# Kernel tuning notes

Measured on AMD Instinct MI355X. Metric: run time of the kernel, lower is better.

## Reference

```python
import jax, jax.numpy as jnp
import numpy as np
import math

V = 1_000_000  # number of mesh vertices
J = 23         # number of joints (fixed by kintree_table in source)
PARENTS = np.array([-1, 0, 1, 1, 3, 4, 5, 4, 7, 4, 9, 1, 11, 12, 13, 12, 15, 12, 17, 0, 19, 0, 21])


def setup_inputs() -> dict:
    key = jax.random.key(0)
    ks = jax.random.split(key, 16)
    v_template = jax.random.normal(ks[0], (1, V, 3), jnp.float32) * 0.5
    w = jax.random.uniform(ks[1], (1, V, J), jnp.float32)
    skinning = w / w.sum(-1, keepdims=True)  # rows sum to 1 like LBS weights
    joints_rest = jax.random.normal(ks[2], (1, J, 3), jnp.float32) * 0.3
    jp = lambda i: jax.random.normal(ks[3 + i], (1, 3), jnp.float32) * 0.1
    return {
        'v_template': v_template,
        'skinning': skinning,
        'joints_rest': joints_rest,
        'joint_0': jp(0), 'joint_1': jp(1), 'joint_2': jp(2), 'joint_3': jp(3),
        'joint_4': jp(4), 'joint_5': jp(5), 'joint_12': jp(6), 'joint_13': jp(7),
        'local_adjust': jax.random.normal(ks[11], (1, V, 3), jnp.float32) * 0.01,
        'displacement': jax.random.normal(ks[12], (1, 1, 3), jnp.float32) * 0.01,
        'scale': jnp.ones((1,), jnp.float32),
        'estimated_location': jax.random.normal(ks[13], (1, 3), jnp.float32),
        'batch_size': 4,
    }


def rodrigues(r):
    # r: [J,3] axis-angle -> [J,3,3] rotation matrices
    angle = jnp.sqrt(jnp.sum(r * r, axis=-1, keepdims=True) + 1e-12)  # [J,1]
    axis = r / angle
    x, y, z = axis[:, 0], axis[:, 1], axis[:, 2]
    zero = jnp.zeros_like(x)
    K = jnp.stack([zero, -z, y, z, zero, -x, -y, x, zero], axis=-1).reshape(-1, 3, 3)
    s = jnp.sin(angle)[..., None]
    c = jnp.cos(angle)[..., None]
    I = jnp.eye(3, dtype=r.dtype)
    return I + s * K + (1.0 - c) * (K @ K)


def build_pose_tensor(joint_0, joint_1, joint_2, joint_3, joint_4, joint_5, joint_12, joint_13):
    pi = math.pi
    pose = jnp.zeros((J, 3), jnp.float32)
    pose = pose.at[0].set(pi / 2 * jnp.tanh(joint_0[0]))
    pose = pose.at[1].set(pi / 4 * jnp.tanh(joint_1[0]))
    pose = pose.at[2].set(pi / 9 * jnp.tanh(joint_2[0]))
    pose = pose.at[3].set(pi / 3 * jnp.tanh(joint_3[0]))
    pose = pose.at[11].set(pi / 3 * jnp.tanh(joint_3[0]) * jnp.array([1.0, -1.0, -1.0], jnp.float32))
    pose = pose.at[4].set(pi / 3 * jnp.tanh(joint_4[0]))
    pose = pose.at[12].set(pi / 3 * jnp.tanh(joint_12[0]))
    pose = pose.at[13].set(pi / 3 * jnp.tanh(joint_13[0]))
    pose = pose.at[5].set(pi / 3 * jnp.tanh(joint_5[0]))
    return pose


def lbs(verts, joints, pose):
    # verts: [V,3], joints: [J,3], pose: [J,3] axis-angle
    R = rodrigues(pose)  # [J,3,3]
    rel = joints.at[1:].add(-joints[PARENTS[1:]])  # parent-relative joint offsets
    # local 4x4 transforms
    T_local = jnp.zeros((J, 4, 4), verts.dtype)
    T_local = T_local.at[:, :3, :3].set(R)
    T_local = T_local.at[:, :3, 3].set(rel)
    T_local = T_local.at[:, 3, 3].set(1.0)
    # compose along kinematic tree (fixed 23-joint chain -> small static loop)
    G = [T_local[0]]
    for j in range(1, J):
        G.append(G[PARENTS[j]] @ T_local[j])
    G = jnp.stack(G)  # [J,4,4]
    posed_joints = G[:, :3, 3]
    # remove rest-pose joint locations: A = G * [[I,-j],[0,1]]
    t_corr = jnp.einsum('jab,jb->ja', G[:, :3, :3], joints)
    A = G.at[:, :3, 3].add(-t_corr)  # [J,4,4]
    # skin vertices: per-vertex blended transform
    T = (skinning_ref[0] @ A.reshape(J, 16)).reshape(-1, 4, 4) if False else None
    return A, posed_joints


def reference(v_template, skinning, joints_rest, joint_0, joint_1, joint_2, joint_3,
              joint_4, joint_5, joint_12, joint_13, local_adjust, displacement,
              scale, estimated_location, batch_size):
    pose = build_pose_tensor(joint_0, joint_1, joint_2, joint_3, joint_4, joint_5,
                             joint_12, joint_13)
    verts = v_template[0] + 0.1 * jnp.tanh(local_adjust[0])  # [V,3]
    joints = joints_rest[0]  # [J,3]
    A, posed_joints = lbs(verts, joints, pose)
    # weighted per-vertex transforms: [V,J] @ [J,16] -> [V,4,4]  (memory-bound)
    Tv = (skinning[0] @ A.reshape(J, 16)).reshape(-1, 4, 4)
    v_h = jnp.concatenate([verts, jnp.ones((verts.shape[0], 1), verts.dtype)], axis=-1)
    verts_posed = jnp.einsum('vab,vb->va', Tv, v_h)[:, :3]  # [V,3]
    disp = 0.1 * jnp.tanh(displacement[0, 0])  # [3]
    loc = estimated_location[0]  # [3]
    verts_out = 0.0035 * scale[0] * verts_posed + loc + disp  # [V,3]
    joints_out = 0.0035 * scale[0] * posed_joints + loc + disp  # [J,3]
    verts_batched = jnp.broadcast_to(verts_out[None], (batch_size,) + verts_out.shape)
    return verts_batched, pose, joints_out, scale, displacement, local_adjust
```

## Files before the change

kernel.cpp:

```cpp
#include <hip/hip_runtime.h>

#define V_N 1000000
#define J_N 23
#define BLK 256

#define OUT_POSE   12000000
#define OUT_JOINTS 12000069
#define OUT_SCALE  12000138
#define OUT_DISP   12000139
#define OUT_LA     12000142

__device__ __constant__ int c_parents[J_N] = {
    -1, 0, 1, 1, 3, 4, 5, 4, 7, 4, 9, 1, 11, 12, 13, 12, 15, 12, 17, 0, 19, 0, 21
};

__global__ void stage1_kernel(
    const float* __restrict__ joints_rest,
    const float* __restrict__ j0, const float* __restrict__ j1,
    const float* __restrict__ j2, const float* __restrict__ j3,
    const float* __restrict__ j4, const float* __restrict__ j5,
    const float* __restrict__ j12, const float* __restrict__ j13,
    const float* __restrict__ disp, const float* __restrict__ scale,
    const float* __restrict__ loc,
    float* __restrict__ wsA, float* __restrict__ out)
{
    __shared__ float jr[J_N][3];
    __shared__ float pose[J_N][3];
    __shared__ float R[J_N][9];
    __shared__ float rel[J_N][3];
    __shared__ float G[J_N][12];
    __shared__ float sb[4];
    const int t = threadIdx.x;

    if (t < J_N * 3) {
        ((float*)jr)[t]   = joints_rest[t];
        ((float*)pose)[t] = 0.0f;
    }
    __syncthreads();

    if (t < 27) {
        const float PI = 3.14159265358979323846f;
        const int   rows[9] = { 0, 1, 2, 3, 11, 4, 5, 12, 13 };
        const float cf[9]   = { PI/2, PI/4, PI/9, PI/3, PI/3, PI/3, PI/3, PI/3, PI/3 };
        int i = t / 3, cmp = t % 3;
        const float* srcs[9];
        srcs[0]=j0; srcs[1]=j1; srcs[2]=j2; srcs[3]=j3; srcs[4]=j3;
        srcs[5]=j4; srcs[6]=j5; srcs[7]=j12; srcs[8]=j13;
        float syz = (rows[i] == 11 && cmp > 0) ? -1.0f : 1.0f;
        pose[rows[i]][cmp] = cf[i] * syz * tanhf(srcs[i][cmp]);
    }
    if (t == 32) {
        sb[0] = 0.0035f * scale[0];
        sb[1] = loc[0] + 0.1f * tanhf(disp[0]);
        sb[2] = loc[1] + 0.1f * tanhf(disp[1]);
        sb[3] = loc[2] + 0.1f * tanhf(disp[2]);
    }
    __syncthreads();

    if (t < J_N) {
        float rx = pose[t][0], ry = pose[t][1], rz = pose[t][2];
        float ang = sqrtf(rx*rx + ry*ry + rz*rz + 1e-12f);
        float inv = 1.0f / ang;
        float x = rx * inv, y = ry * inv, z = rz * inv;
        float s = sinf(ang), c = cosf(ang);
        float K[9]  = { 0.f, -z, y,  z, 0.f, -x,  -y, x, 0.f };
        float K2[9];
        for (int r = 0; r < 3; r++)
            for (int cc = 0; cc < 3; cc++) {
                float a = 0.f;
                for (int k = 0; k < 3; k++) a += K[r*3+k] * K[k*3+cc];
                K2[r*3+cc] = a;
            }
        for (int r = 0; r < 3; r++)
            for (int cc = 0; cc < 3; cc++) {
                float id = (r == cc) ? 1.f : 0.f;
                R[t][r*3+cc] = id + s * K[r*3+cc] + (1.f - c) * K2[r*3+cc];
            }
        int p = c_parents[t];
        for (int cc = 0; cc < 3; cc++)
            rel[t][cc] = (p < 0) ? jr[t][cc] : (jr[t][cc] - jr[p][cc]);
    }
    __syncthreads();

    if (t == 0) {
        for (int r = 0; r < 3; r++) {
            for (int cc = 0; cc < 3; cc++) G[0][r*4+cc] = R[0][r*3+cc];
            G[0][r*4+3] = rel[0][r];
        }
        for (int j = 1; j < J_N; j++) {
            int p = c_parents[j];
            for (int r = 0; r < 3; r++) {
                float g0 = G[p][r*4+0], g1 = G[p][r*4+1], g2 = G[p][r*4+2], g3 = G[p][r*4+3];
                for (int cc = 0; cc < 3; cc++)
                    G[j][r*4+cc] = g0*R[j][0*3+cc] + g1*R[j][1*3+cc] + g2*R[j][2*3+cc];
                G[j][r*4+3] = g0*rel[j][0] + g1*rel[j][1] + g2*rel[j][2] + g3;
            }
        }
    }
    __syncthreads();

    if (t < J_N) {
        for (int r = 0; r < 3; r++) {
            float tc = G[t][r*4+0]*jr[t][0] + G[t][r*4+1]*jr[t][1] + G[t][r*4+2]*jr[t][2];
            wsA[t*12 + r*4 + 0] = G[t][r*4+0];
            wsA[t*12 + r*4 + 1] = G[t][r*4+1];
            wsA[t*12 + r*4 + 2] = G[t][r*4+2];
            wsA[t*12 + r*4 + 3] = G[t][r*4+3] - tc;
            out[OUT_JOINTS + t*3 + r] = sb[0] * G[t][r*4+3] + sb[1+r];
        }
    }
    if (t < J_N * 3) out[OUT_POSE + t] = ((const float*)pose)[t];
    if (t == 0) {
        wsA[276] = sb[0]; wsA[277] = sb[1]; wsA[278] = sb[2]; wsA[279] = sb[3];
        out[OUT_SCALE]  = scale[0];
        out[OUT_DISP+0] = disp[0]; out[OUT_DISP+1] = disp[1]; out[OUT_DISP+2] = disp[2];
    }
}

__global__ void stage2_kernel(
    const float* __restrict__ vt,
    const float* __restrict__ skin,
    const float* __restrict__ la,
    const float* __restrict__ wsA,
    const int* __restrict__ bsp,
    float* __restrict__ out)
{
    const int v = blockIdx.x * BLK + threadIdx.x;
    if (v >= V_N) return;

    const float* wp = skin + (size_t)v * J_N;
    float w[J_N];
    #pragma unroll
    for (int j = 0; j < J_N; j++) w[j] = wp[j];

    const float* vp = vt + (size_t)v * 3;
    const float* lp = la + (size_t)v * 3;
    const float cvx = vp[0], cvy = vp[1], cvz = vp[2];
    const float clx = lp[0], cly = lp[1], clz = lp[2];

    const float vx = cvx + 0.1f * tanhf(clx);
    const float vy = cvy + 0.1f * tanhf(cly);
    const float vz = cvz + 0.1f * tanhf(clz);

    float acc[12];
    #pragma unroll
    for (int k = 0; k < 12; k++) acc[k] = 0.f;
    #pragma unroll
    for (int j = 0; j < J_N; j++) {
        const float wj = w[j];
        const float* Aj = wsA + j * 12;
        #pragma unroll
        for (int k = 0; k < 12; k++) acc[k] = fmaf(wj, Aj[k], acc[k]);
    }

    const float px = acc[0]*vx + acc[1]*vy + acc[2]*vz  + acc[3];
    const float py = acc[4]*vx + acc[5]*vy + acc[6]*vz  + acc[7];
    const float pz = acc[8]*vx + acc[9]*vy + acc[10]*vz + acc[11];
    const float sc = wsA[276];
    const float ox = fmaf(sc, px, wsA[277]);
    const float oy = fmaf(sc, py, wsA[278]);
    const float oz = fmaf(sc, pz, wsA[279]);

    const int bsz = bsp[0];
    float* ob = out + (size_t)v * 3;
    for (int b = 0; b < bsz; b++) {
        ob[0] = ox; ob[1] = oy; ob[2] = oz;
        ob += 3000000;
    }
    float* oe = out + OUT_LA + (size_t)v * 3;
    oe[0] = clx; oe[1] = cly; oe[2] = clz;
}

extern "C" void kernel_launch(void* const* d_in, const int* in_sizes, int n_in,
                              void* d_out, int out_size, void* d_ws, size_t ws_size,
                              hipStream_t stream) {
    const float* vt   = (const float*)d_in[0];
    const float* skin = (const float*)d_in[1];
    const float* jr   = (const float*)d_in[2];
    const float* j0   = (const float*)d_in[3];
    const float* j1   = (const float*)d_in[4];
    const float* j2   = (const float*)d_in[5];
    const float* j3   = (const float*)d_in[6];
    const float* j4   = (const float*)d_in[7];
    const float* j5   = (const float*)d_in[8];
    const float* j12  = (const float*)d_in[9];
    const float* j13  = (const float*)d_in[10];
    const float* la   = (const float*)d_in[11];
    const float* disp = (const float*)d_in[12];
    const float* sc   = (const float*)d_in[13];
    const float* loc  = (const float*)d_in[14];
    const int* bs     = (const int*)d_in[15];

    float* wsA = (float*)d_ws;
    float* out = (float*)d_out;

    stage1_kernel<<<1, 128, 0, stream>>>(jr, j0, j1, j2, j3, j4, j5, j12, j13,
                                         disp, sc, loc, wsA, out);
    stage2_kernel<<<(V_N + BLK - 1) / BLK, BLK, 0, stream>>>(vt, skin, la, wsA, bs, out);
}
```

Before: 216.0 us.

## Stage skinning weights through LDS with coalesced 16-byte loads

The per-vertex kernel now uses 64-thread blocks that cooperatively load the block's contiguous skinning-weight rows as uint4 vectors into shared memory, then each thread reads its own 23 weights from LDS. Before, each thread read its own row of 23 floats with stride-23 access, which coalesces poorly. The change adds a barrier and LDS traffic with bank conflicts from the stride-23 reads, and it relies on V being an exact multiple of 64 since the bounds check was removed.

```diff
diff --git a/kernel.cpp b/kernel.cpp
--- a/kernel.cpp
+++ b/kernel.cpp
@@ -2,7 +2,8 @@
 
 #define V_N 1000000
 #define J_N 23
-#define BLK 256
+#define BLK2 64
+#define NBLK 15625
 
 #define OUT_POSE   12000000
 #define OUT_JOINTS 12000069
@@ -125,34 +126,49 @@
     const int* __restrict__ bsp,
     float* __restrict__ out)
 {
-    const int v = blockIdx.x * BLK + threadIdx.x;
-    if (v >= V_N) return;
-
-    const float* wp = skin + (size_t)v * J_N;
-    float w[J_N];
-    #pragma unroll
-    for (int j = 0; j < J_N; j++) w[j] = wp[j];
+    __shared__ uint4 s_sk[368];
+
+    const int lane = threadIdx.x;
+    const int blk  = blockIdx.x;
+    const int v    = blk * BLK2 + lane;
+
+    const uint4* g = (const uint4*)skin + (size_t)blk * 368;
+    uint4 r0 = g[lane];
+    uint4 r1 = g[lane + 64];
+    uint4 r2 = g[lane + 128];
+    uint4 r3 = g[lane + 192];
+    uint4 r4 = g[lane + 256];
+    uint4 r5 = make_uint4(0u, 0u, 0u, 0u);
+    if (lane < 48) r5 = g[lane + 320];
 
     const float* vp = vt + (size_t)v * 3;
     const float* lp = la + (size_t)v * 3;
     const float cvx = vp[0], cvy = vp[1], cvz = vp[2];
     const float clx = lp[0], cly = lp[1], clz = lp[2];
 
-    const float vx = cvx + 0.1f * tanhf(clx);
-    const float vy = cvy + 0.1f * tanhf(cly);
-    const float vz = cvz + 0.1f * tanhf(clz);
-
+    s_sk[lane]       = r0;
+    s_sk[lane + 64]  = r1;
+    s_sk[lane + 128] = r2;
+    s_sk[lane + 192] = r3;
+    s_sk[lane + 256] = r4;
+    if (lane < 48) s_sk[lane + 320] = r5;
+    __syncthreads();
+
+    const float* wr = (const float*)s_sk + lane * J_N;
     float acc[12];
     #pragma unroll
     for (int k = 0; k < 12; k++) acc[k] = 0.f;
     #pragma unroll
     for (int j = 0; j < J_N; j++) {
-        const float wj = w[j];
+        const float wj = wr[j];
         const float* Aj = wsA + j * 12;
         #pragma unroll
         for (int k = 0; k < 12; k++) acc[k] = fmaf(wj, Aj[k], acc[k]);
     }
 
+    const float vx = cvx + 0.1f * tanhf(clx);
+    const float vy = cvy + 0.1f * tanhf(cly);
+    const float vz = cvz + 0.1f * tanhf(clz);
     const float px = acc[0]*vx + acc[1]*vy + acc[2]*vz  + acc[3];
     const float py = acc[4]*vx + acc[5]*vy + acc[6]*vz  + acc[7];
     const float pz = acc[8]*vx + acc[9]*vy + acc[10]*vz + acc[11];
@@ -196,5 +212,5 @@
 
     stage1_kernel<<<1, 128, 0, stream>>>(jr, j0, j1, j2, j3, j4, j5, j12, j13,
                                          disp, sc, loc, wsA, out);
-    stage2_kernel<<<(V_N + BLK - 1) / BLK, BLK, 0, stream>>>(vt, skin, la, wsA, bs, out);
+    stage2_kernel<<<NBLK, BLK2, 0, stream>>>(vt, skin, la, wsA, bs, out);
 }
```

Result: no change. 220.1 us (+1.9%).

## Process four vertices per thread with 128-bit vector loads and nontemporal stores

Applied to the files above, without the earlier changes.

Each thread now handles four consecutive vertices. That lets it read the 92 skinning weights as 23 aligned uint4 loads, and the vertex and adjustment data as three float4 loads each. Outputs go out as vectorized nontemporal stores, 16-byte for the batched vertices and 8-byte for the local_adjust copy. The aim is fewer memory instructions and better coalescing in a kernel bound by memory bandwidth. The cost is many more registers per thread (92 weights), which lowers occupancy, and per-thread loads of 368 contiguous bytes that are strided across lanes, which may coalesce worse.

```diff
diff --git a/kernel.cpp b/kernel.cpp
--- a/kernel.cpp
+++ b/kernel.cpp
@@ -3,12 +3,16 @@
 #define V_N 1000000
 #define J_N 23
 #define BLK 256
+#define NBLK 977
 
 #define OUT_POSE   12000000
 #define OUT_JOINTS 12000069
 #define OUT_SCALE  12000138
 #define OUT_DISP   12000139
 #define OUT_LA     12000142
+
+typedef float v4f __attribute__((ext_vector_type(4)));
+typedef float v2f __attribute__((ext_vector_type(2)));
 
 __device__ __constant__ int c_parents[J_N] = {
     -1, 0, 1, 1, 3, 4, 5, 4, 7, 4, 9, 1, 11, 12, 13, 12, 15, 12, 17, 0, 19, 0, 21
@@ -125,50 +129,82 @@
     const int* __restrict__ bsp,
     float* __restrict__ out)
 {
-    const int v = blockIdx.x * BLK + threadIdx.x;
-    if (v >= V_N) return;
-
-    const float* wp = skin + (size_t)v * J_N;
-    float w[J_N];
+    const int gid = blockIdx.x * BLK + threadIdx.x;
+    const int v4  = gid << 2;
+    if (v4 >= V_N) return;
+
+    const uint4* g = (const uint4*)skin + (size_t)gid * 23;
+    uint4 wq[23];
     #pragma unroll
-    for (int j = 0; j < J_N; j++) w[j] = wp[j];
-
-    const float* vp = vt + (size_t)v * 3;
-    const float* lp = la + (size_t)v * 3;
-    const float cvx = vp[0], cvy = vp[1], cvz = vp[2];
-    const float clx = lp[0], cly = lp[1], clz = lp[2];
-
-    const float vx = cvx + 0.1f * tanhf(clx);
-    const float vy = cvy + 0.1f * tanhf(cly);
-    const float vz = cvz + 0.1f * tanhf(clz);
-
-    float acc[12];
+    for (int m = 0; m < 23; m++) wq[m] = g[m];
+
+    const float4* vp = (const float4*)(vt + (size_t)v4 * 3);
+    const float4* lp = (const float4*)(la + (size_t)v4 * 3);
+    float4 va = vp[0], vb = vp[1], vc = vp[2];
+    float4 lA = lp[0], lB = lp[1], lC = lp[2];
+
+    const float sc = wsA[276];
+    const float bx = wsA[277], by = wsA[278], bz = wsA[279];
+    const int   bsz = bsp[0];
+
+    float vv[12], ll[12];
+    vv[0]=va.x; vv[1]=va.y; vv[2] =va.z; vv[3] =va.w;
+    vv[4]=vb.x; vv[5]=vb.y; vv[6] =vb.z; vv[7] =vb.w;
+    vv[8]=vc.x; vv[9]=vc.y; vv[10]=vc.z; vv[11]=vc.w;
+    ll[0]=lA.x; ll[1]=lA.y; ll[2] =lA.z; ll[3] =lA.w;
+    ll[4]=lB.x; ll[5]=lB.y; ll[6] =lB.z; ll[7] =lB.w;
+    ll[8]=lC.x; ll[9]=lC.y; ll[10]=lC.z; ll[11]=lC.w;
+
+    const float* wf = (const float*)wq;
+
+    float o[12];
     #pragma unroll
-    for (int k = 0; k < 12; k++) acc[k] = 0.f;
-    #pragma unroll
-    for (int j = 0; j < J_N; j++) {
-        const float wj = w[j];
-        const float* Aj = wsA + j * 12;
+    for (int v = 0; v < 4; v++) {
+        float acc[12];
         #pragma unroll
-        for (int k = 0; k < 12; k++) acc[k] = fmaf(wj, Aj[k], acc[k]);
-    }
-
-    const float px = acc[0]*vx + acc[1]*vy + acc[2]*vz  + acc[3];
-    const float py = acc[4]*vx + acc[5]*vy + acc[6]*vz  + acc[7];
-    const float pz = acc[8]*vx + acc[9]*vy + acc[10]*vz + acc[11];
-    const float sc = wsA[276];
-    const float ox = fmaf(sc, px, wsA[277]);
-    const float oy = fmaf(sc, py, wsA[278]);
-    const float oz = fmaf(sc, pz, wsA[279]);
-
-    const int bsz = bsp[0];
-    float* ob = out + (size_t)v * 3;
+        for (int k = 0; k < 12; k++) acc[k] = 0.f;
+        #pragma unroll
+        for (int j = 0; j < J_N; j++) {
+            const float wj = wf[v * J_N + j];
+            const float* Aj = wsA + j * 12;
+            #pragma unroll
+            for (int k = 0; k < 12; k++) acc[k] = fmaf(wj, Aj[k], acc[k]);
+        }
+        const float vx = vv[v*3+0] + 0.1f * tanhf(ll[v*3+0]);
+        const float vy = vv[v*3+1] + 0.1f * tanhf(ll[v*3+1]);
+        const float vz = vv[v*3+2] + 0.1f * tanhf(ll[v*3+2]);
+        const float px = acc[0]*vx + acc[1]*vy + acc[2]*vz  + acc[3];
+        const float py = acc[4]*vx + acc[5]*vy + acc[6]*vz  + acc[7];
+        const float pz = acc[8]*vx + acc[9]*vy + acc[10]*vz + acc[11];
+        o[v*3+0] = fmaf(sc, px, bx);
+        o[v*3+1] = fmaf(sc, py, by);
+        o[v*3+2] = fmaf(sc, pz, bz);
+    }
+
+    v4f s0 = { o[0], o[1], o[2],  o[3] };
+    v4f s1 = { o[4], o[5], o[6],  o[7] };
+    v4f s2 = { o[8], o[9], o[10], o[11] };
     for (int b = 0; b < bsz; b++) {
-        ob[0] = ox; ob[1] = oy; ob[2] = oz;
-        ob += 3000000;
-    }
-    float* oe = out + OUT_LA + (size_t)v * 3;
-    oe[0] = clx; oe[1] = cly; oe[2] = clz;
+        v4f* ob = (v4f*)(out + (size_t)b * 3000000u + (size_t)v4 * 3);
+        __builtin_nontemporal_store(s0, ob + 0);
+        __builtin_nontemporal_store(s1, ob + 1);
+        __builtin_nontemporal_store(s2, ob + 2);
+    }
+    {
+        v2f* oe = (v2f*)((char*)out + 48000568ull + (size_t)v4 * 12u);
+        v2f e0 = { ll[0],  ll[1]  };
+        v2f e1 = { ll[2],  ll[3]  };
+        v2f e2 = { ll[4],  ll[5]  };
+        v2f e3 = { ll[6],  ll[7]  };
+        v2f e4 = { ll[8],  ll[9]  };
+        v2f e5 = { ll[10], ll[11] };
+        __builtin_nontemporal_store(e0, oe + 0);
+        __builtin_nontemporal_store(e1, oe + 1);
+        __builtin_nontemporal_store(e2, oe + 2);
+        __builtin_nontemporal_store(e3, oe + 3);
+        __builtin_nontemporal_store(e4, oe + 4);
+        __builtin_nontemporal_store(e5, oe + 5);
+    }
 }
 
 extern "C" void kernel_launch(void* const* d_in, const int* in_sizes, int n_in,
@@ -196,5 +232,5 @@
 
     stage1_kernel<<<1, 128, 0, stream>>>(jr, j0, j1, j2, j3, j4, j5, j12, j13,
                                          disp, sc, loc, wsA, out);
-    stage2_kernel<<<(V_N + BLK - 1) / BLK, BLK, 0, stream>>>(vt, skin, la, wsA, bs, out);
+    stage2_kernel<<<NBLK, BLK, 0, stream>>>(vt, skin, la, wsA, bs, out);
 }
```

New measurement: 240.5 us. +11.4%, slower.

## Stage skinning weights through LDS with coalesced nontemporal 16-byte loads

Applied to the files above, without the earlier changes.

The skinning matrix tile for each block (256 vertices x 23 weights) is now loaded cooperatively as 16-byte vectors with nontemporal hints into shared memory, then each thread reads its 23 weights from LDS. Before, each thread read its row with a stride of 23 floats, so accesses were uncoalesced and wasted bandwidth. This costs about 23 KB of LDS per block, which may limit occupancy, and a block-wide barrier. The 23-float row stride in LDS can also cause bank conflicts.

```diff
diff --git a/kernel.cpp b/kernel.cpp
--- a/kernel.cpp
+++ b/kernel.cpp
@@ -3,12 +3,15 @@
 #define V_N 1000000
 #define J_N 23
 #define BLK 256
+#define NFULL 3906
 
 #define OUT_POSE   12000000
 #define OUT_JOINTS 12000069
 #define OUT_SCALE  12000138
 #define OUT_DISP   12000139
 #define OUT_LA     12000142
+
+typedef unsigned int v4u __attribute__((ext_vector_type(4)));
 
 __device__ __constant__ int c_parents[J_N] = {
     -1, 0, 1, 1, 3, 4, 5, 4, 7, 4, 9, 1, 11, 12, 13, 12, 15, 12, 17, 0, 19, 0, 21
@@ -125,50 +128,80 @@
     const int* __restrict__ bsp,
     float* __restrict__ out)
 {
-    const int v = blockIdx.x * BLK + threadIdx.x;
-    if (v >= V_N) return;
-
-    const float* wp = skin + (size_t)v * J_N;
-    float w[J_N];
-    #pragma unroll
-    for (int j = 0; j < J_N; j++) w[j] = wp[j];
-
-    const float* vp = vt + (size_t)v * 3;
-    const float* lp = la + (size_t)v * 3;
-    const float cvx = vp[0], cvy = vp[1], cvz = vp[2];
-    const float clx = lp[0], cly = lp[1], clz = lp[2];
-
-    const float vx = cvx + 0.1f * tanhf(clx);
-    const float vy = cvy + 0.1f * tanhf(cly);
-    const float vz = cvz + 0.1f * tanhf(clz);
-
-    float acc[12];
-    #pragma unroll
-    for (int k = 0; k < 12; k++) acc[k] = 0.f;
-    #pragma unroll
-    for (int j = 0; j < J_N; j++) {
-        const float wj = w[j];
-        const float* Aj = wsA + j * 12;
+    __shared__ v4u s_sk[1472];
+
+    const int tid = threadIdx.x;
+    const int blk = blockIdx.x;
+    const int v0  = blk * BLK;
+    const int v   = v0 + tid;
+
+    const v4u* g = (const v4u*)skin + (size_t)blk * 1472;
+
+    float cvx = 0.f, cvy = 0.f, cvz = 0.f, clx = 0.f, cly = 0.f, clz = 0.f;
+
+    if (blk < NFULL) {
+        v4u r0 = __builtin_nontemporal_load(g + tid);
+        v4u r1 = __builtin_nontemporal_load(g + tid + 256);
+        v4u r2 = __builtin_nontemporal_load(g + tid + 512);
+        v4u r3 = __builtin_nontemporal_load(g + tid + 768);
+        v4u r4 = __builtin_nontemporal_load(g + tid + 1024);
+        v4u r5 = (v4u){0u, 0u, 0u, 0u};
+        if (tid < 192) r5 = __builtin_nontemporal_load(g + tid + 1280);
+        const float* vp = vt + (size_t)v * 3;
+        const float* lp = la + (size_t)v * 3;
+        cvx = vp[0]; cvy = vp[1]; cvz = vp[2];
+        clx = lp[0]; cly = lp[1]; clz = lp[2];
+
+        s_sk[tid]        = r0;
+        s_sk[tid + 256]  = r1;
+        s_sk[tid + 512]  = r2;
+        s_sk[tid + 768]  = r3;
+        s_sk[tid + 1024] = r4;
+        if (tid < 192) s_sk[tid + 1280] = r5;
+    } else {
+        for (int i = tid; i < 368; i += BLK)
+            s_sk[i] = __builtin_nontemporal_load(g + i);
+        if (v < V_N) {
+            const float* vp = vt + (size_t)v * 3;
+            const float* lp = la + (size_t)v * 3;
+            cvx = vp[0]; cvy = vp[1]; cvz = vp[2];
+            clx = lp[0]; cly = lp[1]; clz = lp[2];
+        }
+    }
+    __syncthreads();
+
+    if (v < V_N) {
+        const float* wr = (const float*)s_sk + tid * J_N;
+        float acc[12];
         #pragma unroll
-        for (int k = 0; k < 12; k++) acc[k] = fmaf(wj, Aj[k], acc[k]);
-    }
-
-    const float px = acc[0]*vx + acc[1]*vy + acc[2]*vz  + acc[3];
-    const float py = acc[4]*vx + acc[5]*vy + acc[6]*vz  + acc[7];
-    const float pz = acc[8]*vx + acc[9]*vy + acc[10]*vz + acc[11];
-    const float sc = wsA[276];
-    const float ox = fmaf(sc, px, wsA[277]);
-    const float oy = fmaf(sc, py, wsA[278]);
-    const float oz = fmaf(sc, pz, wsA[279]);
-
-    const int bsz = bsp[0];
-    float* ob = out + (size_t)v * 3;
-    for (int b = 0; b < bsz; b++) {
-        ob[0] = ox; ob[1] = oy; ob[2] = oz;
-        ob += 3000000;
-    }
-    float* oe = out + OUT_LA + (size_t)v * 3;
-    oe[0] = clx; oe[1] = cly; oe[2] = clz;
+        for (int k = 0; k < 12; k++) acc[k] = 0.f;
+        #pragma unroll
+        for (int j = 0; j < J_N; j++) {
+            const float wj = wr[j];
+            const float* Aj = wsA + j * 12;
+            #pragma unroll
+            for (int k = 0; k < 12; k++) acc[k] = fmaf(wj, Aj[k], acc[k]);
+        }
+        const float vx = cvx + 0.1f * tanhf(clx);
+        const float vy = cvy + 0.1f * tanhf(cly);
+        const float vz = cvz + 0.1f * tanhf(clz);
+        const float px = acc[0]*vx + acc[1]*vy + acc[2]*vz  + acc[3];
+        const float py = acc[4]*vx + acc[5]*vy + acc[6]*vz  + acc[7];
+        const float pz = acc[8]*vx + acc[9]*vy + acc[10]*vz + acc[11];
+        const float sc = wsA[276];
+        const float ox = fmaf(sc, px, wsA[277]);
+        const float oy = fmaf(sc, py, wsA[278]);
+        const float oz = fmaf(sc, pz, wsA[279]);
+
+        const int bsz = bsp[0];
+        float* ob = out + (size_t)v * 3;
+        for (int b = 0; b < bsz; b++) {
+            ob[0] = ox; ob[1] = oy; ob[2] = oz;
+            ob += 3000000;
+        }
+        float* oe = out + OUT_LA + (size_t)v * 3;
+        oe[0] = clx; oe[1] = cly; oe[2] = clz;
+    }
 }
 
 extern "C" void kernel_launch(void* const* d_in, const int* in_sizes, int n_in,
```

New measurement: 213.3 us. About the same (-1.2%).
